# Kernel tuning notes

Measured on AMD Instinct MI355X. Metric: run time of the kernel, lower is better.

The kernel has to match this reference:

```python
import jax, jax.numpy as jnp
import numpy as np

DIM = 1024
N_HEADS = 16
HEAD_DIM = DIM // N_HEADS
SCALE = HEAD_DIM ** -0.5


def setup_inputs() -> dict:
    key = jax.random.key(0)
    k1, k2, k3 = jax.random.split(key, 3)
    inp = jax.random.normal(k1, (8, 1024, DIM), dtype=jnp.float32)
    w_qkv = jax.random.normal(k2, (DIM, 3 * DIM), dtype=jnp.float32) * 0.02
    b_qkv = jnp.zeros((3 * DIM,), dtype=jnp.float32)
    w_proj = jax.random.normal(k3, (DIM, DIM), dtype=jnp.float32) * 0.02
    b_proj = jnp.zeros((DIM,), dtype=jnp.float32)
    return {"inp": inp, "w_qkv": w_qkv, "b_qkv": b_qkv, "w_proj": w_proj, "b_proj": b_proj}


def reference(inp, w_qkv, b_qkv, w_proj, b_proj):
    B, N, D = inp.shape
    qkv = inp @ w_qkv + b_qkv                      # [B, N, 3D]
    qkv = qkv.reshape(B, N, 3, N_HEADS, HEAD_DIM)
    qkv = jnp.transpose(qkv, (2, 0, 3, 1, 4))      # [3, B, H, N, hd]
    q, k, v = qkv[0], qkv[1], qkv[2]
    scores = jnp.einsum('bhqd,bhkd->bhqk', q, k) * SCALE
    attn = jax.nn.softmax(scores, axis=-1)         # dropout p=0 -> identity
    out = jnp.einsum('bhqk,bhkd->bhqd', attn, v)   # [B, H, N, hd]
    out = jnp.transpose(out, (0, 2, 1, 3)).reshape(B, N, D)
    return out @ w_proj + b_proj
```

## Files before the change

kernel.cpp:

```cpp
#include <hip/hip_runtime.h>
#include <hip/hip_bf16.h>
#include <cstdint>


typedef __attribute__((ext_vector_type(8))) short short8;
typedef __attribute__((ext_vector_type(4))) float floatx4;
typedef __attribute__((ext_vector_type(16))) float f32x16;
typedef __attribute__((ext_vector_type(2))) unsigned int uint2v;

__device__ __forceinline__ ushort f2bf(float f) {
    union { float f; uint32_t i; } v; v.f = f;
    uint32_t r = v.i + 0x7fffu + ((v.i >> 16) & 1u);
    return (ushort)(r >> 16);
}
__device__ __forceinline__ uint32_t pack2(float a, float b) {
    return (uint32_t)f2bf(a) | ((uint32_t)f2bf(b) << 16);
}
__device__ __forceinline__ uint32_t cvtpk_bf16(float a, float b) {
    uint32_t r;
    asm("v_cvt_pk_bf16_f32 %0, %1, %2" : "=v"(r) : "v"(a), "v"(b));
    return r;
}
__device__ __forceinline__ void gl2lds16(const void* g, void* lds) {
    __builtin_amdgcn_global_load_lds(
        (const __attribute__((address_space(1))) uint32_t*)(uintptr_t)g,
        (__attribute__((address_space(3))) uint32_t*)(uintptr_t)lds,
        16, 0, 0);
}

__global__ __launch_bounds__(256)
void prep_fused(const float* __restrict__ in, ushort* __restrict__ ob,
                const float* __restrict__ W, ushort* __restrict__ WT,
                int nA) {
    __shared__ ushort T[64 * 72];
    const int tid = threadIdx.x;
    int bx = blockIdx.x;
    if (bx < nA) {
        const int i = (bx * 256 + tid) * 8;
        const float4 f0 = *(const float4*)&in[i];
        const float4 f1 = *(const float4*)&in[i + 4];
        uint4 pk;
        pk.x = pack2(f0.x, f0.y); pk.y = pack2(f0.z, f0.w);
        pk.z = pack2(f1.x, f1.y); pk.w = pack2(f1.z, f1.w);
        *(uint4*)&ob[i] = pk;
        return;
    }
    bx -= nA;
    const int K = 1024, N = 3072;
    const int k0 = (bx / 48) * 64, n0 = (bx % 48) * 64;
#pragma unroll
    for (int i = 0; i < 4; ++i) {
        int c = tid + i * 256;
        int kl = c >> 4, n4 = (c & 15) << 2;
        const float4 f = *(const float4*)&W[(size_t)(k0 + kl) * N + n0 + n4];
        T[(n4 + 0) * 72 + kl] = f2bf(f.x);
        T[(n4 + 1) * 72 + kl] = f2bf(f.y);
        T[(n4 + 2) * 72 + kl] = f2bf(f.z);
        T[(n4 + 3) * 72 + kl] = f2bf(f.w);
    }
    __syncthreads();
#pragma unroll
    for (int i = 0; i < 2; ++i) {
        int c = tid + i * 256;
        int nl = c >> 3, k8 = (c & 7) << 3;
        *(uint4*)&WT[(size_t)(n0 + nl) * K + k0 + k8] =
            *(const uint4*)&T[nl * 72 + k8];
    }
}

__global__ __launch_bounds__(256)
void wprep(const float* __restrict__ W, ushort* __restrict__ WT,
           int K, int N) {
    __shared__ ushort T[64 * 72];
    const int tid = threadIdx.x;
    const int k0 = blockIdx.y * 64, n0 = blockIdx.x * 64;
#pragma unroll
    for (int i = 0; i < 4; ++i) {
        int c = tid + i * 256;
        int kl = c >> 4, n4 = (c & 15) << 2;
        const float4 f = *(const float4*)&W[(size_t)(k0 + kl) * N + n0 + n4];
        T[(n4 + 0) * 72 + kl] = f2bf(f.x);
        T[(n4 + 1) * 72 + kl] = f2bf(f.y);
        T[(n4 + 2) * 72 + kl] = f2bf(f.z);
        T[(n4 + 3) * 72 + kl] = f2bf(f.w);
    }
    __syncthreads();
#pragma unroll
    for (int i = 0; i < 2; ++i) {
        int c = tid + i * 256;
        int nl = c >> 3, k8 = (c & 7) << 3;
        *(uint4*)&WT[(size_t)(n0 + nl) * K + k0 + k8] =
            *(const uint4*)&T[nl * 72 + k8];
    }
}

template <int MODE, typename OutT>
__global__ __launch_bounds__(256)
void gemm_bt(const ushort* __restrict__ A, const ushort* __restrict__ BT,
             const float* __restrict__ bias, OutT* __restrict__ C,
             ushort* __restrict__ qb, ushort* __restrict__ kb,
             ushort* __restrict__ vb, int M, int Nn, int K) {
    __shared__ ushort As[128 * 64];
    __shared__ ushort Bs[128 * 64];
    const int tid = threadIdx.x;
    const int lane = tid & 63, w = tid >> 6;
    const int wm = w & 1, wn = w >> 1;
    const int l16 = lane & 15, quad = lane >> 4;
    const int m0 = blockIdx.y * 128, n0 = blockIdx.x * 128;
    const int srow = lane >> 3;
    const int cg = (lane & 7) ^ srow;
    const int sx = l16 & 7;

    floatx4 acc[4][4];
#pragma unroll
    for (int i = 0; i < 4; ++i)
#pragma unroll
        for (int j = 0; j < 4; ++j) acc[i][j] = (floatx4)0.f;

    const int nkt = K >> 6;
    for (int kt = 0; kt < nkt; ++kt) {
        __syncthreads();
#pragma unroll
        for (int i = 0; i < 4; ++i) {
            const int row = w * 32 + i * 8 + srow;
            gl2lds16(&BT[(size_t)(n0 + row) * K + kt * 64 + cg * 8],
                     &Bs[(w * 32 + i * 8) * 64]);
            gl2lds16(&A[(size_t)(m0 + row) * K + kt * 64 + cg * 8],
                     &As[(w * 32 + i * 8) * 64]);
        }
        __syncthreads();
#pragma unroll
        for (int kk = 0; kk < 2; ++kk) {
            const int sl = ((kk << 2) | quad) ^ sx;
            short8 af[4], bfr[4];
#pragma unroll
            for (int mi = 0; mi < 4; ++mi)
                af[mi] = *(const short8*)&As[(wm * 64 + mi * 16 + l16) * 64 +
                                             sl * 8];
#pragma unroll
            for (int ni = 0; ni < 4; ++ni)
                bfr[ni] = *(const short8*)&Bs[(wn * 64 + ni * 16 + l16) * 64 +
                                              sl * 8];
#pragma unroll
            for (int mi = 0; mi < 4; ++mi)
#pragma unroll
                for (int ni = 0; ni < 4; ++ni)
                    acc[mi][ni] = __builtin_amdgcn_mfma_f32_16x16x32_bf16(
                        af[mi], bfr[ni], acc[mi][ni], 0, 0, 0);
        }
    }

#pragma unroll
    for (int mi = 0; mi < 4; ++mi) {
#pragma unroll
        for (int ni = 0; ni < 4; ++ni) {
            const int jg = n0 + wn * 64 + ni * 16 + l16;
            const float bv = bias[jg];
#pragma unroll
            for (int r = 0; r < 4; ++r) {
                const int mg = m0 + wm * 64 + mi * 16 + quad * 4 + r;
                const float vout = acc[mi][ni][r] + bv;
                if (MODE == 0) {
                    if (sizeof(OutT) == 4)
                        ((float*)C)[(size_t)mg * Nn + jg] = vout;
                    else
                        ((ushort*)C)[(size_t)mg * Nn + jg] = f2bf(vout);
                } else {
                    const int which = jg >> 10;
                    const int h = (jg & 1023) >> 6;
                    const int d = jg & 63;
                    const int bb = mg >> 10, nn = mg & 1023;
                    if (which == 0)
                        qb[(size_t)((bb * 16 + h) * 1024 + nn) * 64 + d] =
                            f2bf(vout);
                    else if (which == 1)
                        kb[(size_t)((bb * 16 + h) * 1024 + nn) * 64 + d] =
                            f2bf(vout);
                    else
                        vb[((size_t)(bb * 16 + h) * 64 + d) * 1024 + nn] =
                            f2bf(vout);
                }
            }
        }
    }
}

__global__ __launch_bounds__(256, 4)
void attn_kernel(const ushort* __restrict__ q, const ushort* __restrict__ k,
                 const ushort* __restrict__ v, ushort* __restrict__ o) {
    __shared__ ushort Qs[128 * 64];
    __shared__ ushort Ks[64 * 64];
    __shared__ ushort VTs[64 * 64];
    const int tid = threadIdx.x;
    const int lane = tid & 63, w = tid >> 6;
    const int l31 = lane & 31, hi = lane >> 5, l7 = lane & 7;
    const int h = blockIdx.x, qt = blockIdx.y, b = blockIdx.z;
    const size_t head_off = (size_t)(b * 16 + h) * 1024 * 64;
    const ushort* Qp = q + head_off + (size_t)qt * 128 * 64;
    const ushort* Vp = v + head_off;
    const int srow = lane >> 3;
    const int cg = (lane & 7) ^ srow;
    const float CEXP = 0.125f * 1.44269504f;

#pragma unroll
    for (int g = 0; g < 4; ++g)
        gl2lds16(&Qp[(size_t)(w * 32 + g * 8 + srow) * 64 + cg * 8],
                 &Qs[(w * 32 + g * 8) * 64]);
    __syncthreads();

    short8 bq[4];
#pragma unroll
    for (int c = 0; c < 4; ++c)
        bq[c] = *(const short8*)&Qs[(w * 32 + l31) * 64 +
                                    ((2 * c + hi) ^ l7) * 8];

    f32x16 oacc[2];
    oacc[0] = (f32x16)0.f;
    oacc[1] = (f32x16)0.f;
    float ls = 0.f;

    for (int kt = 0; kt < 16; ++kt) {
        __syncthreads();
        const ushort* Kp = k + head_off + (size_t)kt * 64 * 64;
#pragma unroll
        for (int g = 0; g < 2; ++g) {
            gl2lds16(&Kp[(size_t)(w * 16 + g * 8 + srow) * 64 + cg * 8],
                     &Ks[(w * 16 + g * 8) * 64]);
            gl2lds16(&Vp[(size_t)(w * 16 + g * 8 + srow) * 1024 +
                         kt * 64 + cg * 8],
                     &VTs[(w * 16 + g * 8) * 64]);
        }
        __syncthreads();

#pragma unroll
        for (int st = 0; st < 2; ++st) {
            f32x16 sacc = (f32x16)0.f;
            __builtin_amdgcn_s_setprio(1);
#pragma unroll
            for (int c = 0; c < 4; ++c) {
                short8 ak = *(const short8*)&Ks[(st * 32 + l31) * 64 +
                                                ((2 * c + hi) ^ l7) * 8];
                sacc = __builtin_amdgcn_mfma_f32_32x32x16_bf16(
                    ak, bq[c], sacc, 0, 0, 0);
            }
            __builtin_amdgcn_s_setprio(0);
            uint32_t wd[8];
#pragma unroll
            for (int i = 0; i < 8; ++i) {
                const float e0 = __builtin_amdgcn_exp2f(sacc[2 * i] * CEXP);
                const float e1 = __builtin_amdgcn_exp2f(sacc[2 * i + 1] * CEXP);
                ls += e0 + e1;
                wd[i] = cvtpk_bf16(e0, e1);
            }
            short8 ap[2];
#pragma unroll
            for (int c2 = 0; c2 < 2; ++c2) {
                uint2v sA = __builtin_amdgcn_permlane32_swap(
                    wd[4 * c2 + 0], wd[4 * c2 + 2], false, false);
                uint2v sB = __builtin_amdgcn_permlane32_swap(
                    wd[4 * c2 + 1], wd[4 * c2 + 3], false, false);
                union { uint32_t u[4]; short8 s; } t;
                t.u[0] = sA[0]; t.u[1] = sB[0];
                t.u[2] = sA[1]; t.u[3] = sB[1];
                ap[c2] = t.s;
            }
            __builtin_amdgcn_s_setprio(1);
#pragma unroll
            for (int dt = 0; dt < 2; ++dt)
#pragma unroll
                for (int c2 = 0; c2 < 2; ++c2) {
                    short8 bv = *(const short8*)&VTs[
                        (dt * 32 + l31) * 64 +
                        ((st * 4 + c2 * 2 + hi) ^ l7) * 8];
                    oacc[dt] = __builtin_amdgcn_mfma_f32_32x32x16_bf16(
                        ap[c2], bv, oacc[dt], 0, 0, 0);
                }
            __builtin_amdgcn_s_setprio(0);
        }
    }

    ls += __shfl_xor(ls, 32, 64);
    const float inv = 1.f / ls;

#pragma unroll
    for (int r = 0; r < 16; ++r) {
        const int qout = (r & 3) + ((r >> 2) << 3) + (hi << 2);
        const float iq = __shfl(inv, qout, 64);
        const int n = qt * 128 + w * 32 + qout;
#pragma unroll
        for (int dt = 0; dt < 2; ++dt)
            o[((size_t)(b * 1024 + n)) * 1024 + h * 64 + dt * 32 + l31] =
                f2bf(oacc[dt][r] * iq);
    }
}

extern "C" void kernel_launch(void* const* d_in, const int* in_sizes, int n_in,
                              void* d_out, int out_size, void* d_ws,
                              size_t ws_size, hipStream_t stream) {
    const void *inp = d_in[0], *w_qkv = d_in[1], *b_qkv = d_in[2],
               *w_proj = d_in[3], *b_proj = d_in[4];
    for (int i = 0; i < n_in; ++i) {
        switch (in_sizes[i]) {
            case 8 * 1024 * 1024: inp    = d_in[i]; break;
            case 3 * 1024 * 1024: w_qkv  = d_in[i]; break;
            case 3072:            b_qkv  = d_in[i]; break;
            case 1024 * 1024:     w_proj = d_in[i]; break;
            case 1024:            b_proj = d_in[i]; break;
        }
    }
    float* out = (float*)d_out;

    char* ws = (char*)d_ws;
    ushort* qb  = (ushort*)(ws);
    ushort* kb  = (ushort*)(ws + (size_t)16 * 1024 * 1024);
    ushort* vbT = (ushort*)(ws + (size_t)32 * 1024 * 1024);
    ushort* ob  = (ushort*)(ws + (size_t)48 * 1024 * 1024);
    ushort* wqkvT  = ob;
    ushort* wprojT = qb;
    ushort* abf = (ushort*)d_out;

    prep_fused<<<4096 + 768, 256, 0, stream>>>(
        (const float*)inp, abf, (const float*)w_qkv, wqkvT, 4096);

    gemm_bt<1, ushort><<<dim3(3072 / 128, 8192 / 128), 256, 0, stream>>>(
        abf, wqkvT, (const float*)b_qkv, (ushort*)nullptr, qb, kb, vbT,
        8192, 3072, 1024);

    attn_kernel<<<dim3(16, 8, 8), 256, 0, stream>>>(qb, kb, vbT, ob);

    wprep<<<dim3(1024 / 64, 1024 / 64), 256, 0, stream>>>(
        (const float*)w_proj, wprojT, 1024, 1024);

    gemm_bt<0, float><<<dim3(1024 / 128, 8192 / 128), 256, 0, stream>>>(
        ob, wprojT, (const float*)b_proj, out, nullptr, nullptr, nullptr,
        8192, 1024, 1024);
}
```

Measured before the change: 255.5 us.

## Double-buffer K/V tiles in attention and swizzle GEMM block order

The attention kernel now prefetches the next K/V tile into a second LDS buffer while the current tile is being computed. The Q staging area is reused as one of the ping-pong buffers, so the tile loop needs one barrier per iteration instead of two. Separately, the GEMM kernel remaps its block IDs so consecutive workgroups are spread across strided groups, which is meant to improve cache locality across XCDs. LDS use stays at 32KB, but correctness now depends on the single barrier and on completion of the async global-to-LDS loads.

```diff
diff --git a/kernel.cpp b/kernel.cpp
--- a/kernel.cpp
+++ b/kernel.cpp
@@ -106,7 +106,11 @@
     const int lane = tid & 63, w = tid >> 6;
     const int wm = w & 1, wn = w >> 1;
     const int l16 = lane & 15, quad = lane >> 4;
-    const int m0 = blockIdx.y * 128, n0 = blockIdx.x * 128;
+    const int nwg = gridDim.x * gridDim.y;
+    int id = blockIdx.y * gridDim.x + blockIdx.x;
+    id = (id & 7) * (nwg >> 3) + (id >> 3);
+    const int bx = id % gridDim.x, by = id / gridDim.x;
+    const int m0 = by * 128, n0 = bx * 128;
     const int srow = lane >> 3;
     const int cg = (lane & 7) ^ srow;
     const int sx = l16 & 7;
@@ -188,15 +192,16 @@
 __global__ __launch_bounds__(256, 4)
 void attn_kernel(const ushort* __restrict__ q, const ushort* __restrict__ k,
                  const ushort* __restrict__ v, ushort* __restrict__ o) {
-    __shared__ ushort Qs[128 * 64];
-    __shared__ ushort Ks[64 * 64];
-    __shared__ ushort VTs[64 * 64];
+    __shared__ ushort SM[16384];
+    ushort* bufA = SM;
+    ushort* bufB = SM + 8192;
     const int tid = threadIdx.x;
     const int lane = tid & 63, w = tid >> 6;
     const int l31 = lane & 31, hi = lane >> 5, l7 = lane & 7;
     const int h = blockIdx.x, qt = blockIdx.y, b = blockIdx.z;
     const size_t head_off = (size_t)(b * 16 + h) * 1024 * 64;
     const ushort* Qp = q + head_off + (size_t)qt * 128 * 64;
+    const ushort* Kbase = k + head_off;
     const ushort* Vp = v + head_off;
     const int srow = lane >> 3;
     const int cg = (lane & 7) ^ srow;
@@ -205,14 +210,22 @@
 #pragma unroll
     for (int g = 0; g < 4; ++g)
         gl2lds16(&Qp[(size_t)(w * 32 + g * 8 + srow) * 64 + cg * 8],
-                 &Qs[(w * 32 + g * 8) * 64]);
+                 &bufA[(w * 32 + g * 8) * 64]);
+#pragma unroll
+    for (int g = 0; g < 2; ++g) {
+        gl2lds16(&Kbase[(size_t)(w * 16 + g * 8 + srow) * 64 + cg * 8],
+                 &bufB[(w * 16 + g * 8) * 64]);
+        gl2lds16(&Vp[(size_t)(w * 16 + g * 8 + srow) * 1024 + cg * 8],
+                 &bufB[4096 + (w * 16 + g * 8) * 64]);
+    }
     __syncthreads();
 
     short8 bq[4];
 #pragma unroll
     for (int c = 0; c < 4; ++c)
-        bq[c] = *(const short8*)&Qs[(w * 32 + l31) * 64 +
-                                    ((2 * c + hi) ^ l7) * 8];
+        bq[c] = *(const short8*)&bufA[(w * 32 + l31) * 64 +
+                                      ((2 * c + hi) ^ l7) * 8];
+    __syncthreads();
 
     f32x16 oacc[2];
     oacc[0] = (f32x16)0.f;
@@ -220,17 +233,21 @@
     float ls = 0.f;
 
     for (int kt = 0; kt < 16; ++kt) {
-        __syncthreads();
-        const ushort* Kp = k + head_off + (size_t)kt * 64 * 64;
-#pragma unroll
-        for (int g = 0; g < 2; ++g) {
-            gl2lds16(&Kp[(size_t)(w * 16 + g * 8 + srow) * 64 + cg * 8],
-                     &Ks[(w * 16 + g * 8) * 64]);
-            gl2lds16(&Vp[(size_t)(w * 16 + g * 8 + srow) * 1024 +
-                         kt * 64 + cg * 8],
-                     &VTs[(w * 16 + g * 8) * 64]);
-        }
-        __syncthreads();
+        ushort* cur = (kt & 1) ? bufA : bufB;
+        ushort* nxt = (kt & 1) ? bufB : bufA;
+        if (kt < 15) {
+            const ushort* Kp = Kbase + (size_t)(kt + 1) * 64 * 64;
+#pragma unroll
+            for (int g = 0; g < 2; ++g) {
+                gl2lds16(&Kp[(size_t)(w * 16 + g * 8 + srow) * 64 + cg * 8],
+                         &nxt[(w * 16 + g * 8) * 64]);
+                gl2lds16(&Vp[(size_t)(w * 16 + g * 8 + srow) * 1024 +
+                             (kt + 1) * 64 + cg * 8],
+                         &nxt[4096 + (w * 16 + g * 8) * 64]);
+            }
+        }
+        const ushort* Ks = cur;
+        const ushort* VTs = cur + 4096;
 
 #pragma unroll
         for (int st = 0; st < 2; ++st) {
@@ -277,6 +294,7 @@
                 }
             __builtin_amdgcn_s_setprio(0);
         }
+        __syncthreads();
     }
 
     ls += __shfl_xor(ls, 32, 64);
```

After: 250.5 us. -2.0%, faster.
